# Kernel optimization log

Measured on AMD Instinct MI355X. Metric: run time of the kernel, lower is better.

## Reference

```python
import jax, jax.numpy as jnp
import numpy as np

E, H, DEPTH, V, B, T = 512, 512, 2, 32000, 64, 32


def setup_inputs() -> dict:
    key = jax.random.key(0)
    ks = jax.random.split(key, 16)
    s = 1.0 / np.sqrt(H)
    inp = {
        "sentence": jax.random.randint(ks[0], (B, T), 0, V),
        "features": jax.random.normal(ks[1], (B, E), dtype=jnp.float32),
        "lengths": jax.random.randint(ks[2], (B,), 1, T),
        "emb": jax.random.normal(ks[3], (V, E), dtype=jnp.float32),
        "W_ih0": jax.random.uniform(ks[4], (4 * H, E), minval=-s, maxval=s),
        "W_hh0": jax.random.uniform(ks[5], (4 * H, H), minval=-s, maxval=s),
        "b_ih0": jax.random.uniform(ks[6], (4 * H,), minval=-s, maxval=s),
        "b_hh0": jax.random.uniform(ks[7], (4 * H,), minval=-s, maxval=s),
        "W_ih1": jax.random.uniform(ks[8], (4 * H, H), minval=-s, maxval=s),
        "W_hh1": jax.random.uniform(ks[9], (4 * H, H), minval=-s, maxval=s),
        "b_ih1": jax.random.uniform(ks[10], (4 * H,), minval=-s, maxval=s),
        "b_hh1": jax.random.uniform(ks[11], (4 * H,), minval=-s, maxval=s),
        "fc_W": jax.random.uniform(ks[12], (V, H), minval=-s, maxval=s),
        "fc_b": jax.random.uniform(ks[13], (V,), minval=-s, maxval=s),
    }
    return inp


def _lstm_layer(x, W_ih, W_hh, b_ih, b_hh):
    # x: [B, T, in]; PyTorch gate order i, f, g, o. Zero initial (h, c).
    b, t, _ = x.shape
    h_dim = W_hh.shape[1]
    xp = jnp.einsum('bti,gi->btg', x, W_ih) + b_ih + b_hh  # [B, T, 4H]
    h0 = jnp.zeros((b, h_dim), x.dtype)
    c0 = jnp.zeros((b, h_dim), x.dtype)

    def step(carry, xt):
        h, c = carry
        gates = xt + h @ W_hh.T
        i, f, g, o = jnp.split(gates, 4, axis=-1)
        i = jax.nn.sigmoid(i)
        f = jax.nn.sigmoid(f)
        g = jnp.tanh(g)
        o = jax.nn.sigmoid(o)
        c = f * c + i * g
        h = o * jnp.tanh(c)
        return (h, c), h

    _, hs = jax.lax.scan(step, (h0, c0), xp.transpose(1, 0, 2))  # [T, B, H]
    return hs.transpose(1, 0, 2)


def reference(sentence, features, lengths, emb, W_ih0, W_hh0, b_ih0, b_hh0,
              W_ih1, W_hh1, b_ih1, b_hh1, fc_W, fc_b):
    embeds = emb[sentence]  # [B, T, E]
    # LSTM inputs: features first, then embeds[:, :-1] (teacher forcing)
    x = jnp.concatenate([features[:, None, :], embeds[:, :-1, :]], axis=1)
    h = _lstm_layer(x, W_ih0, W_hh0, b_ih0, b_hh0)
    h = _lstm_layer(h, W_ih1, W_hh1, b_ih1, b_hh1)
    fc_out = jnp.einsum('bth,vh->btv', h, fc_W) + fc_b  # [B, T, V]
    return fc_out.transpose(0, 2, 1)  # [B, V, T]
```

## Files before the change

kernel.cpp:

```cpp
#include <hip/hip_runtime.h>
#include <math.h>

#define E_DIM 512
#define H_DIM 512
#define V_DIM 32000
#define B_DIM 64
#define T_DIM 32

__global__ __launch_bounds__(128) void build_x(const int* __restrict__ sent,
                                               const float* __restrict__ feat,
                                               const float* __restrict__ emb,
                                               float* __restrict__ x0) {
    int m = blockIdx.x;
    int b = m >> 5, t = m & 31;
    const float* src = (t == 0) ? (feat + b * E_DIM)
                                : (emb + (long long)sent[b * T_DIM + t - 1] * E_DIM);
    float4 v = ((const float4*)src)[threadIdx.x];
    ((float4*)(x0 + (size_t)m * E_DIM))[threadIdx.x] = v;
}

template <int MODE>
__global__ __launch_bounds__(256) void gemm128(const float* __restrict__ A,
                                               const float* __restrict__ Bw,
                                               const float* __restrict__ bias1,
                                               const float* __restrict__ bias2,
                                               float* __restrict__ C, int N_) {
    __shared__ float As[16][129];
    __shared__ float Bs[16][129];
    const int tid = threadIdx.x;
    const int tx = tid & 15, ty = tid >> 4;
    const int mtile = blockIdx.x * 128, ntile = blockIdx.y * 128;
    const int mi = MODE ? tx : ty;
    const int ni = MODE ? ty : tx;
    float acc[8][8] = {};
    const int lcol = tid & 15;
    const int lrow = tid >> 4;

    for (int kc = 0; kc < 512; kc += 16) {
#pragma unroll
        for (int rr = 0; rr < 8; ++rr) {
            int row = lrow + 16 * rr;
            As[lcol][row] = A[(size_t)(mtile + row) * 512 + kc + lcol];
            Bs[lcol][row] = Bw[(size_t)(ntile + row) * 512 + kc + lcol];
        }
        __syncthreads();
#pragma unroll
        for (int k = 0; k < 16; ++k) {
            float a[8], bfr[8];
#pragma unroll
            for (int i = 0; i < 8; ++i) a[i] = As[k][mi + 16 * i];
#pragma unroll
            for (int j = 0; j < 8; ++j) bfr[j] = Bs[k][ni + 16 * j];
#pragma unroll
            for (int i = 0; i < 8; ++i)
#pragma unroll
                for (int j = 0; j < 8; ++j) acc[i][j] += a[i] * bfr[j];
        }
        __syncthreads();
    }

    if (MODE == 0) {
#pragma unroll
        for (int i = 0; i < 8; ++i) {
            int m = mtile + mi + 16 * i;
#pragma unroll
            for (int j = 0; j < 8; ++j) {
                int n = ntile + ni + 16 * j;
                C[(size_t)m * N_ + n] = acc[i][j] + bias1[n] + bias2[n];
            }
        }
    } else {
#pragma unroll
        for (int i = 0; i < 8; ++i) {
            int m = mtile + mi + 16 * i;
            int b = m >> 5, t = m & 31;
#pragma unroll
            for (int j = 0; j < 8; ++j) {
                int v = ntile + ni + 16 * j;
                C[(size_t)(b * V_DIM + v) * T_DIM + t] = acc[i][j] + bias1[v];
            }
        }
    }
}

__global__ __launch_bounds__(256) void lstm_step(const float* __restrict__ xp,
                                                 const float* __restrict__ Whh,
                                                 const float* __restrict__ h_in,
                                                 float* __restrict__ h_out,
                                                 float* __restrict__ cbuf,
                                                 float* __restrict__ hs,
                                                 int t) {
    __shared__ float h_s[16][36];
    __shared__ float W_s[64][36];
    const int tid = threadIdx.x;
    const int bb = tid >> 4, jj = tid & 15;
    const int b0 = blockIdx.x * 16;
    const int j0 = blockIdx.y * 16;
    float acc[4] = {0.f, 0.f, 0.f, 0.f};

    for (int kc = 0; kc < 512; kc += 32) {
        {
            int r = tid >> 5, col = tid & 31;
            h_s[r][col]     = h_in[(b0 + r) * 512 + kc + col];
            h_s[r + 8][col] = h_in[(b0 + r + 8) * 512 + kc + col];
        }
#pragma unroll
        for (int i = 0; i < 8; ++i) {
            int idx = tid + i * 256;
            int r = idx >> 5, col = idx & 31;
            int n = (r >> 4) * 512 + j0 + (r & 15);
            W_s[r][col] = Whh[(size_t)n * 512 + kc + col];
        }
        __syncthreads();
#pragma unroll
        for (int k4 = 0; k4 < 8; ++k4) {
            float4 hv = *(const float4*)&h_s[bb][k4 * 4];
#pragma unroll
            for (int q = 0; q < 4; ++q) {
                float4 wv = *(const float4*)&W_s[q * 16 + jj][k4 * 4];
                acc[q] += hv.x * wv.x + hv.y * wv.y + hv.z * wv.z + hv.w * wv.w;
            }
        }
        __syncthreads();
    }

    const int b = b0 + bb, j = j0 + jj;
    const float* xrow = xp + (size_t)(b * T_DIM + t) * 2048;
    float gi = acc[0] + xrow[j];
    float gf = acc[1] + xrow[512 + j];
    float gg = acc[2] + xrow[1024 + j];
    float go = acc[3] + xrow[1536 + j];
    float si = 1.f / (1.f + expf(-gi));
    float sf = 1.f / (1.f + expf(-gf));
    float tg = tanhf(gg);
    float so = 1.f / (1.f + expf(-go));
    int idx = b * 512 + j;
    float cv = sf * cbuf[idx] + si * tg;
    cbuf[idx] = cv;
    float hv = so * tanhf(cv);
    h_out[idx] = hv;
    hs[(size_t)(b * T_DIM + t) * 512 + j] = hv;
}

extern "C" void kernel_launch(void* const* d_in, const int* in_sizes, int n_in,
                              void* d_out, int out_size, void* d_ws, size_t ws_size,
                              hipStream_t stream) {
    const int*   sent  = (const int*)d_in[0];
    const float* feat  = (const float*)d_in[1];
    const float* emb   = (const float*)d_in[3];
    const float* W_ih0 = (const float*)d_in[4];
    const float* W_hh0 = (const float*)d_in[5];
    const float* b_ih0 = (const float*)d_in[6];
    const float* b_hh0 = (const float*)d_in[7];
    const float* W_ih1 = (const float*)d_in[8];
    const float* W_hh1 = (const float*)d_in[9];
    const float* b_ih1 = (const float*)d_in[10];
    const float* b_hh1 = (const float*)d_in[11];
    const float* fc_W  = (const float*)d_in[12];
    const float* fc_b  = (const float*)d_in[13];
    float* out = (float*)d_out;
    float* ws  = (float*)d_ws;

    float* x0   = ws;
    float* xp   = ws + 1048576;
    float* hs0  = ws + 5242880;
    float* hs1  = ws + 6291456;
    float* ha   = ws + 7340032;
    float* cbuf = ws + 7372800;
    float* hb   = ws + 7405568;

    build_x<<<dim3(2048), dim3(128), 0, stream>>>(sent, feat, emb, x0);

    gemm128<0><<<dim3(16, 16), dim3(256), 0, stream>>>(x0, W_ih0, b_ih0, b_hh0, xp, 2048);
    hipMemsetAsync(ha, 0, 2 * 32768 * sizeof(float), stream);
    {
        float* hin = ha; float* hout = hb;
        for (int t = 0; t < T_DIM; ++t) {
            lstm_step<<<dim3(4, 32), dim3(256), 0, stream>>>(xp, W_hh0, hin, hout, cbuf, hs0, t);
            float* tmp = hin; hin = hout; hout = tmp;
        }
    }

    gemm128<0><<<dim3(16, 16), dim3(256), 0, stream>>>(hs0, W_ih1, b_ih1, b_hh1, xp, 2048);
    hipMemsetAsync(ha, 0, 2 * 32768 * sizeof(float), stream);
    {
        float* hin = ha; float* hout = hb;
        for (int t = 0; t < T_DIM; ++t) {
            lstm_step<<<dim3(4, 32), dim3(256), 0, stream>>>(xp, W_hh1, hin, hout, cbuf, hs1, t);
            float* tmp = hin; hin = hout; hout = tmp;
        }
    }

    gemm128<1><<<dim3(16, 250), dim3(256), 0, stream>>>(hs1, fc_W, fc_b, nullptr, out, V_DIM);
}
```

Baseline: 2.996 ms.

## Fuse both LSTM layers into a persistent cooperative kernel and use fp16 MFMA

Replaces the 64 per-timestep LSTM launches with one cooperative persistent kernel. It keeps W_hh slices resident in LDS and pipelines layer 1 one step behind layer 0, with a grid sync between steps. The layer-1 input projection is computed per step with fp16 MFMA instead of a separate GEMM. The final FC projection is rewritten to use fp16 MFMA with vectorized output stores. This removes launch overhead and repeated weight reloads, at the cost of fp16 precision loss and grid-wide synchronization latency.

```diff
diff --git a/kernel.cpp b/kernel.cpp
--- a/kernel.cpp
+++ b/kernel.cpp
@@ -1,5 +1,12 @@
 #include <hip/hip_runtime.h>
+#include <hip/hip_fp16.h>
+#include <hip/hip_cooperative_groups.h>
 #include <math.h>
+
+namespace cg = cooperative_groups;
+
+using half8 = __attribute__((ext_vector_type(8))) _Float16;
+using f32x4 = __attribute__((ext_vector_type(4))) float;
 
 #define E_DIM 512
 #define H_DIM 512
@@ -19,19 +26,17 @@
     ((float4*)(x0 + (size_t)m * E_DIM))[threadIdx.x] = v;
 }
 
-template <int MODE>
-__global__ __launch_bounds__(256) void gemm128(const float* __restrict__ A,
-                                               const float* __restrict__ Bw,
-                                               const float* __restrict__ bias1,
-                                               const float* __restrict__ bias2,
-                                               float* __restrict__ C, int N_) {
+__global__ __launch_bounds__(256) void gemm128xp(const float* __restrict__ A,
+                                                 const float* __restrict__ Bw,
+                                                 const float* __restrict__ bias1,
+                                                 const float* __restrict__ bias2,
+                                                 float* __restrict__ C) {
     __shared__ float As[16][129];
     __shared__ float Bs[16][129];
     const int tid = threadIdx.x;
     const int tx = tid & 15, ty = tid >> 4;
     const int mtile = blockIdx.x * 128, ntile = blockIdx.y * 128;
-    const int mi = MODE ? tx : ty;
-    const int ni = MODE ? ty : tx;
+    const int mi = ty, ni = tx;
     float acc[8][8] = {};
     const int lcol = tid & 15;
     const int lrow = tid >> 4;
@@ -58,88 +63,224 @@
         }
         __syncthreads();
     }
-
-    if (MODE == 0) {
-#pragma unroll
-        for (int i = 0; i < 8; ++i) {
-            int m = mtile + mi + 16 * i;
-#pragma unroll
-            for (int j = 0; j < 8; ++j) {
-                int n = ntile + ni + 16 * j;
-                C[(size_t)m * N_ + n] = acc[i][j] + bias1[n] + bias2[n];
+#pragma unroll
+    for (int i = 0; i < 8; ++i) {
+        int m = mtile + mi + 16 * i;
+#pragma unroll
+        for (int j = 0; j < 8; ++j) {
+            int n = ntile + ni + 16 * j;
+            C[(size_t)m * 2048 + n] = acc[i][j] + bias1[n] + bias2[n];
+        }
+    }
+}
+
+__global__ __launch_bounds__(256) void f32_to_f16_vec(const float* __restrict__ s,
+                                                      __half* __restrict__ d) {
+    int i = (blockIdx.x * 256 + threadIdx.x) * 4;
+    float4 v = *(const float4*)&s[i];
+    d[i + 0] = __float2half(v.x);
+    d[i + 1] = __float2half(v.y);
+    d[i + 2] = __float2half(v.z);
+    d[i + 3] = __float2half(v.w);
+}
+
+__global__ __launch_bounds__(256) void lstm_persistent(
+    const float* __restrict__ xp0,
+    const float* __restrict__ Whh0,
+    const float* __restrict__ Whh1,
+    const __half* __restrict__ Wih1h,
+    const float* __restrict__ bih1,
+    const float* __restrict__ bhh1,
+    float* __restrict__ h0buf,
+    float* __restrict__ h1buf,
+    __half* __restrict__ hs0h,
+    __half* __restrict__ hs1h)
+{
+    extern __shared__ float lds[];
+    cg::grid_group grid = cg::this_grid();
+    const int wg = blockIdx.x;
+    const int tid = threadIdx.x;
+
+    if (wg < 128) {
+        float(*W)[516] = reinterpret_cast<float(*)[516]>(lds);
+        const int b0 = (wg >> 5) * 16;
+        const int j0 = (wg & 31) * 16;
+        const int bb = tid >> 4, jj = tid & 15;
+        for (int idx = tid; idx < 64 * 128; idx += 256) {
+            int row = idx >> 7, k4 = idx & 127;
+            int grow = (row >> 4) * 512 + j0 + (row & 15);
+            *(float4*)&W[row][k4 * 4] = *(const float4*)&Whh0[(size_t)grow * 512 + k4 * 4];
+        }
+        __syncthreads();
+        const int b = b0 + bb, j = j0 + jj;
+        float creg = 0.f;
+        for (int it = 0; it < 34; ++it) {
+            if (it < 32) {
+                const float* hrow = h0buf + ((it & 1) << 15) + (size_t)b * 512;
+                float a0 = 0.f, a1 = 0.f, a2 = 0.f, a3 = 0.f;
+#pragma unroll 4
+                for (int k4 = 0; k4 < 128; ++k4) {
+                    float4 hv = ((const float4*)hrow)[k4];
+                    float4 w0 = *(const float4*)&W[jj][k4 * 4];
+                    float4 w1 = *(const float4*)&W[16 + jj][k4 * 4];
+                    float4 w2 = *(const float4*)&W[32 + jj][k4 * 4];
+                    float4 w3 = *(const float4*)&W[48 + jj][k4 * 4];
+                    a0 += hv.x * w0.x + hv.y * w0.y + hv.z * w0.z + hv.w * w0.w;
+                    a1 += hv.x * w1.x + hv.y * w1.y + hv.z * w1.z + hv.w * w1.w;
+                    a2 += hv.x * w2.x + hv.y * w2.y + hv.z * w2.z + hv.w * w2.w;
+                    a3 += hv.x * w3.x + hv.y * w3.y + hv.z * w3.z + hv.w * w3.w;
+                }
+                const float* xr = xp0 + ((size_t)b * 32 + it) * 2048 + j;
+                float gi = a0 + xr[0];
+                float gf = a1 + xr[512];
+                float gg = a2 + xr[1024];
+                float go = a3 + xr[1536];
+                float si = 1.f / (1.f + __expf(-gi));
+                float sf = 1.f / (1.f + __expf(-gf));
+                float tg = tanhf(gg);
+                float so = 1.f / (1.f + __expf(-go));
+                creg = sf * creg + si * tg;
+                float hv_ = so * tanhf(creg);
+                h0buf[(((it + 1) & 1) << 15) + b * 512 + j] = hv_;
+                hs0h[((size_t)it * 64 + b) * 512 + j] = __float2half(hv_);
             }
+            if (it < 33) { __threadfence(); grid.sync(); }
         }
     } else {
-#pragma unroll
-        for (int i = 0; i < 8; ++i) {
-            int m = mtile + mi + 16 * i;
-            int b = m >> 5, t = m & 31;
-#pragma unroll
-            for (int j = 0; j < 8; ++j) {
-                int v = ntile + ni + 16 * j;
-                C[(size_t)(b * V_DIM + v) * T_DIM + t] = acc[i][j] + bias1[v];
+        float(*W)[516] = reinterpret_cast<float(*)[516]>(lds);
+        float* xps = lds + 32 * 516;
+        const int idx = wg - 128;
+        const int b0 = (idx >> 6) * 32;
+        const int j0 = (idx & 63) * 8;
+        const int bb = tid >> 3, jj = tid & 7;
+        for (int i2 = tid; i2 < 32 * 128; i2 += 256) {
+            int row = i2 >> 7, k4 = i2 & 127;
+            int grow = (row >> 3) * 512 + j0 + (row & 7);
+            *(float4*)&W[row][k4 * 4] = *(const float4*)&Whh1[(size_t)grow * 512 + k4 * 4];
+        }
+        float bias[4];
+#pragma unroll
+        for (int q = 0; q < 4; ++q) {
+            int n = q * 512 + j0 + jj;
+            bias[q] = bih1[n] + bhh1[n];
+        }
+        const int lane = tid & 63, wv = tid >> 6;
+        const int mh = wv >> 1, nh = wv & 1;
+        const int l15 = lane & 15, lk = (lane >> 4) * 8;
+        const int arow = b0 + mh * 16 + l15;
+        const int nidx = nh * 16 + l15;
+        const int growB = (nidx >> 3) * 512 + j0 + (nidx & 7);
+        const int b = b0 + bb, j = j0 + jj;
+        float creg = 0.f;
+        __syncthreads();
+        for (int it = 0; it < 34; ++it) {
+            if (it >= 1 && it < 33) {
+                const int t1 = it - 1;
+                const __half* hsrc = hs0h + (size_t)t1 * 32768;
+                f32x4 acc = {0.f, 0.f, 0.f, 0.f};
+#pragma unroll
+                for (int kc = 0; kc < 512; kc += 32) {
+                    half8 av = *(const half8*)&hsrc[(size_t)arow * 512 + kc + lk];
+                    half8 bv = *(const half8*)&Wih1h[(size_t)growB * 512 + kc + lk];
+                    acc = __builtin_amdgcn_mfma_f32_16x16x32_f16(av, bv, acc, 0, 0, 0);
+                }
+                float* xb = xps + (it & 1) * (32 * 33);
+#pragma unroll
+                for (int r = 0; r < 4; ++r)
+                    xb[(mh * 16 + (lane >> 4) * 4 + r) * 33 + nidx] = acc[r];
             }
-        }
-    }
-}
-
-__global__ __launch_bounds__(256) void lstm_step(const float* __restrict__ xp,
-                                                 const float* __restrict__ Whh,
-                                                 const float* __restrict__ h_in,
-                                                 float* __restrict__ h_out,
-                                                 float* __restrict__ cbuf,
-                                                 float* __restrict__ hs,
-                                                 int t) {
-    __shared__ float h_s[16][36];
-    __shared__ float W_s[64][36];
+            if (it >= 2) {
+                const int t2 = it - 2;
+                const float* hrow = h1buf + ((it & 1) << 15) + (size_t)b * 512;
+                float a0 = 0.f, a1 = 0.f, a2 = 0.f, a3 = 0.f;
+#pragma unroll 4
+                for (int k4 = 0; k4 < 128; ++k4) {
+                    float4 hv = ((const float4*)hrow)[k4];
+                    float4 w0 = *(const float4*)&W[jj][k4 * 4];
+                    float4 w1 = *(const float4*)&W[8 + jj][k4 * 4];
+                    float4 w2 = *(const float4*)&W[16 + jj][k4 * 4];
+                    float4 w3 = *(const float4*)&W[24 + jj][k4 * 4];
+                    a0 += hv.x * w0.x + hv.y * w0.y + hv.z * w0.z + hv.w * w0.w;
+                    a1 += hv.x * w1.x + hv.y * w1.y + hv.z * w1.z + hv.w * w1.w;
+                    a2 += hv.x * w2.x + hv.y * w2.y + hv.z * w2.z + hv.w * w2.w;
+                    a3 += hv.x * w3.x + hv.y * w3.y + hv.z * w3.z + hv.w * w3.w;
+                }
+                const float* xb = xps + ((it - 1) & 1) * (32 * 33) + bb * 33;
+                float gi = a0 + xb[jj] + bias[0];
+                float gf = a1 + xb[8 + jj] + bias[1];
+                float gg = a2 + xb[16 + jj] + bias[2];
+                float go = a3 + xb[24 + jj] + bias[3];
+                float si = 1.f / (1.f + __expf(-gi));
+                float sf = 1.f / (1.f + __expf(-gf));
+                float tg = tanhf(gg);
+                float so = 1.f / (1.f + __expf(-go));
+                creg = sf * creg + si * tg;
+                float hv_ = so * tanhf(creg);
+                h1buf[(((it + 1) & 1) << 15) + b * 512 + j] = hv_;
+                hs1h[((size_t)b * 32 + t2) * 512 + j] = __float2half(hv_);
+            }
+            if (it < 33) { __threadfence(); grid.sync(); }
+        }
+    }
+}
+
+__global__ __launch_bounds__(256) void fc_mfma(const __half* __restrict__ A,
+                                               const float* __restrict__ Bw,
+                                               const float* __restrict__ bias,
+                                               float* __restrict__ out) {
     const int tid = threadIdx.x;
-    const int bb = tid >> 4, jj = tid & 15;
-    const int b0 = blockIdx.x * 16;
-    const int j0 = blockIdx.y * 16;
-    float acc[4] = {0.f, 0.f, 0.f, 0.f};
+    const int lane = tid & 63, wv = tid >> 6;
+    const int wm = wv >> 1, wn = wv & 1;
+    const int m_base = blockIdx.x * 128 + wm * 64;
+    const int n_base = blockIdx.y * 128 + wn * 64;
+    const int l15 = lane & 15, lk = (lane >> 4) * 8;
+    f32x4 zero = {0.f, 0.f, 0.f, 0.f};
+    f32x4 acc[4][4];
+#pragma unroll
+    for (int i = 0; i < 4; ++i)
+#pragma unroll
+        for (int j2 = 0; j2 < 4; ++j2) acc[i][j2] = zero;
 
     for (int kc = 0; kc < 512; kc += 32) {
-        {
-            int r = tid >> 5, col = tid & 31;
-            h_s[r][col]     = h_in[(b0 + r) * 512 + kc + col];
-            h_s[r + 8][col] = h_in[(b0 + r + 8) * 512 + kc + col];
-        }
-#pragma unroll
-        for (int i = 0; i < 8; ++i) {
-            int idx = tid + i * 256;
-            int r = idx >> 5, col = idx & 31;
-            int n = (r >> 4) * 512 + j0 + (r & 15);
-            W_s[r][col] = Whh[(size_t)n * 512 + kc + col];
-        }
-        __syncthreads();
-#pragma unroll
-        for (int k4 = 0; k4 < 8; ++k4) {
-            float4 hv = *(const float4*)&h_s[bb][k4 * 4];
-#pragma unroll
-            for (int q = 0; q < 4; ++q) {
-                float4 wv = *(const float4*)&W_s[q * 16 + jj][k4 * 4];
-                acc[q] += hv.x * wv.x + hv.y * wv.y + hv.z * wv.z + hv.w * wv.w;
-            }
-        }
-        __syncthreads();
-    }
-
-    const int b = b0 + bb, j = j0 + jj;
-    const float* xrow = xp + (size_t)(b * T_DIM + t) * 2048;
-    float gi = acc[0] + xrow[j];
-    float gf = acc[1] + xrow[512 + j];
-    float gg = acc[2] + xrow[1024 + j];
-    float go = acc[3] + xrow[1536 + j];
-    float si = 1.f / (1.f + expf(-gi));
-    float sf = 1.f / (1.f + expf(-gf));
-    float tg = tanhf(gg);
-    float so = 1.f / (1.f + expf(-go));
-    int idx = b * 512 + j;
-    float cv = sf * cbuf[idx] + si * tg;
-    cbuf[idx] = cv;
-    float hv = so * tanhf(cv);
-    h_out[idx] = hv;
-    hs[(size_t)(b * T_DIM + t) * 512 + j] = hv;
+        half8 a[4], bfr[4];
+#pragma unroll
+        for (int i = 0; i < 4; ++i)
+            a[i] = *(const half8*)&A[(size_t)(m_base + i * 16 + l15) * 512 + kc + lk];
+#pragma unroll
+        for (int j2 = 0; j2 < 4; ++j2) {
+            const float* bp = &Bw[(size_t)(n_base + j2 * 16 + l15) * 512 + kc + lk];
+            float4 x0 = *(const float4*)bp;
+            float4 x1 = *(const float4*)(bp + 4);
+            half8 hb;
+            hb[0] = (_Float16)x0.x; hb[1] = (_Float16)x0.y;
+            hb[2] = (_Float16)x0.z; hb[3] = (_Float16)x0.w;
+            hb[4] = (_Float16)x1.x; hb[5] = (_Float16)x1.y;
+            hb[6] = (_Float16)x1.z; hb[7] = (_Float16)x1.w;
+            bfr[j2] = hb;
+        }
+#pragma unroll
+        for (int i = 0; i < 4; ++i)
+#pragma unroll
+            for (int j2 = 0; j2 < 4; ++j2)
+                acc[i][j2] = __builtin_amdgcn_mfma_f32_16x16x32_f16(a[i], bfr[j2], acc[i][j2], 0, 0, 0);
+    }
+#pragma unroll
+    for (int i = 0; i < 4; ++i) {
+        const int m0 = m_base + i * 16 + (lane >> 4) * 4;
+        const int bq = m0 >> 5;
+        const int t0 = m0 & 31;
+#pragma unroll
+        for (int j2 = 0; j2 < 4; ++j2) {
+            const int v = n_base + j2 * 16 + l15;
+            const float bv = bias[v];
+            float4 o;
+            o.x = acc[i][j2][0] + bv;
+            o.y = acc[i][j2][1] + bv;
+            o.z = acc[i][j2][2] + bv;
+            o.w = acc[i][j2][3] + bv;
+            *(float4*)&out[((size_t)bq * V_DIM + v) * 32 + t0] = o;
+        }
+    }
 }
 
 extern "C" void kernel_launch(void* const* d_in, const int* in_sizes, int n_in,
@@ -161,35 +302,32 @@
     float* out = (float*)d_out;
     float* ws  = (float*)d_ws;
 
-    float* x0   = ws;
-    float* xp   = ws + 1048576;
-    float* hs0  = ws + 5242880;
-    float* hs1  = ws + 6291456;
-    float* ha   = ws + 7340032;
-    float* cbuf = ws + 7372800;
-    float* hb   = ws + 7405568;
+    float*  x0    = ws;
+    float*  xp0   = ws + 1048576;
+    float*  h0buf = ws + 5242880;
+    float*  h1buf = ws + 5308416;
+    __half* hs0h  = (__half*)(ws + 5373952);
+    __half* hs1h  = (__half*)(ws + 5898240);
+    __half* Wih1h = (__half*)(ws + 6422528);
 
     build_x<<<dim3(2048), dim3(128), 0, stream>>>(sent, feat, emb, x0);
-
-    gemm128<0><<<dim3(16, 16), dim3(256), 0, stream>>>(x0, W_ih0, b_ih0, b_hh0, xp, 2048);
-    hipMemsetAsync(ha, 0, 2 * 32768 * sizeof(float), stream);
+    gemm128xp<<<dim3(16, 16), dim3(256), 0, stream>>>(x0, W_ih0, b_ih0, b_hh0, xp0);
+    f32_to_f16_vec<<<dim3(1024), dim3(256), 0, stream>>>(W_ih1, Wih1h);
+    hipMemsetAsync(h0buf, 0, 2 * 65536 * sizeof(float), stream);
+
     {
-        float* hin = ha; float* hout = hb;
-        for (int t = 0; t < T_DIM; ++t) {
-            lstm_step<<<dim3(4, 32), dim3(256), 0, stream>>>(xp, W_hh0, hin, hout, cbuf, hs0, t);
-            float* tmp = hin; hin = hout; hout = tmp;
-        }
-    }
-
-    gemm128<0><<<dim3(16, 16), dim3(256), 0, stream>>>(hs0, W_ih1, b_ih1, b_hh1, xp, 2048);
-    hipMemsetAsync(ha, 0, 2 * 32768 * sizeof(float), stream);
-    {
-        float* hin = ha; float* hout = hb;
-        for (int t = 0; t < T_DIM; ++t) {
-            lstm_step<<<dim3(4, 32), dim3(256), 0, stream>>>(xp, W_hh1, hin, hout, cbuf, hs1, t);
-            float* tmp = hin; hin = hout; hout = tmp;
-        }
-    }
-
-    gemm128<1><<<dim3(16, 250), dim3(256), 0, stream>>>(hs1, fc_W, fc_b, nullptr, out, V_DIM);
-}
+        const float* a0 = xp0;  const float* a1 = W_hh0; const float* a2 = W_hh1;
+        const __half* a3 = Wih1h;
+        const float* a4 = b_ih1; const float* a5 = b_hh1;
+        float* a6 = h0buf; float* a7 = h1buf;
+        __half* a8 = hs0h; __half* a9 = hs1h;
+        void* args[] = {(void*)&a0, (void*)&a1, (void*)&a2, (void*)&a3, (void*)&a4,
+                        (void*)&a5, (void*)&a6, (void*)&a7, (void*)&a8, (void*)&a9};
+        hipFuncSetAttribute(reinterpret_cast<const void*>(lstm_persistent),
+                            hipFuncAttributeMaxDynamicSharedMemorySize, 64 * 516 * 4);
+        hipLaunchCooperativeKernel(lstm_persistent, dim3(256), dim3(256), args,
+                                   (unsigned)(64 * 516 * 4), stream);
+    }
+
+    fc_mfma<<<dim3(16, 250), dim3(256), 0, stream>>>(hs1h, fc_W, fc_b, out);
+}
```

After: 3.094 ms. 1.03x slower.
